# Optimization experiments

Measured on AMD Instinct MI355X. Metric: run time of the kernel, lower is better.

Reference implementation:

```python
import jax, jax.numpy as jnp
import numpy as np


def setup_inputs() -> dict:
    key = jax.random.key(0)
    k1, k2, k3, k4 = jax.random.split(key, 4)
    B, S, d_in, d_out = 4, 2048, 1024, 1024
    scale = 1.0 / np.sqrt(d_in)
    x = jax.random.normal(k1, (B, S, d_in), dtype=jnp.float32)
    # Linear weights stored as [d_in, d_out] so projection is x @ W
    Wq = jax.random.normal(k2, (d_in, d_out), dtype=jnp.float32) * scale
    Wk = jax.random.normal(k3, (d_in, d_out), dtype=jnp.float32) * scale
    Wv = jax.random.normal(k4, (d_in, d_out), dtype=jnp.float32) * scale
    return {"x": x, "Wq": Wq, "Wk": Wk, "Wv": Wv}


def reference(x, Wq, Wk, Wv):
    # QKV projections (no bias, matching qkv_bias=False)
    q = jnp.einsum("bsi,io->bso", x, Wq)
    k = jnp.einsum("bsi,io->bso", x, Wk)
    v = jnp.einsum("bsi,io->bso", x, Wv)
    d_k = k.shape[-1]
    # attn_scores = q @ k^T, causal mask (strict upper triangle -> -inf)
    scores = jnp.einsum("bqd,bkd->bqk", q, k)
    S = scores.shape[-1]
    causal = jnp.tril(jnp.ones((S, S), dtype=bool))  # True where allowed
    scores = jnp.where(causal, scores, -jnp.inf)
    attn = jax.nn.softmax(scores / jnp.sqrt(jnp.asarray(d_k, scores.dtype)), axis=-1)
    # dropout p=0.0 -> identity
    return jnp.einsum("bqk,bkd->bqd", attn, v)
```

## Files before the change

kernel.cpp:

```cpp
#include <hip/hip_runtime.h>

typedef _Float16 half8 __attribute__((ext_vector_type(8)));
typedef _Float16 half4 __attribute__((ext_vector_type(4)));
typedef float f32x4 __attribute__((ext_vector_type(4)));

#define ATT_SCALE 0.03125f
#define S_LEN 2048
#define D_DIM 1024
#define NB 4

__device__ __forceinline__ void async_cp16(const _Float16* g, _Float16* l)
{
    __builtin_amdgcn_global_load_lds(
        (const __attribute__((address_space(1))) void*)g,
        (__attribute__((address_space(3))) void*)l, 16, 0, 0);
}

__device__ __forceinline__ void gemm_core(const _Float16* __restrict__ Ag,
                                          const _Float16* __restrict__ Bg,
                                          int lda, int ldb, int ksteps,
                                          f32x4 acc[4][4])
{
    __shared__ _Float16 As[128 * 32];
    __shared__ _Float16 Bs[128 * 32];

    const int t    = threadIdx.x;
    const int wave = t >> 6;
    const int lane = t & 63;
    const int wm   = (wave >> 1) * 64;
    const int wn   = (wave & 1) * 64;
    const int lg   = lane >> 4;
    const int lr   = lane & 15;

    const int c0 = t,        r0 = c0 >> 2, h0 = (c0 & 3) * 8;
    const int c1 = 256 + t,  r1 = c1 >> 2, h1 = (c1 & 3) * 8;
    const int lb0 = (wave * 64) * 8;
    const int lb1 = (256 + wave * 64) * 8;

    const _Float16* a0p = Ag + (long)r0 * lda + h0;
    const _Float16* a1p = Ag + (long)r1 * lda + h1;
    const _Float16* b0p = Bg + (long)r0 * ldb + h0;
    const _Float16* b1p = Bg + (long)r1 * ldb + h1;

    for (int ks = 0; ks < ksteps; ++ks) {
        __syncthreads();
        async_cp16(a0p, As + lb0);
        async_cp16(a1p, As + lb1);
        async_cp16(b0p, Bs + lb0);
        async_cp16(b1p, Bs + lb1);
        __syncthreads();

        a0p += 32; a1p += 32; b0p += 32; b1p += 32;

        half8 af[4], bf[4];
#pragma unroll
        for (int i = 0; i < 4; ++i)
            af[i] = *(const half8*)&As[(wm + i * 16 + lr) * 32 + lg * 8];
#pragma unroll
        for (int j = 0; j < 4; ++j)
            bf[j] = *(const half8*)&Bs[(wn + j * 16 + lr) * 32 + lg * 8];

#pragma unroll
        for (int i = 0; i < 4; ++i)
#pragma unroll
            for (int j = 0; j < 4; ++j)
                acc[i][j] = __builtin_amdgcn_mfma_f32_16x16x32_f16(af[i], bf[j], acc[i][j], 0, 0, 0);
    }
}

__global__ void zero_sums_kernel(float* __restrict__ rs)
{
    rs[blockIdx.x * 256 + threadIdx.x] = 0.f;
}

__global__ void zero_out_kernel(float4* __restrict__ p, long n4)
{
    const float4 z = {0.f, 0.f, 0.f, 0.f};
    for (long i = (long)blockIdx.x * blockDim.x + threadIdx.x; i < n4;
         i += (long)gridDim.x * blockDim.x)
        p[i] = z;
}

__global__ void cast_x_kernel(const float* __restrict__ X, _Float16* __restrict__ Xh, int n)
{
    int i = blockIdx.x * blockDim.x + threadIdx.x;
    if (i * 4 >= n) return;
    float4 v = ((const float4*)X)[i];
    half4 h;
    h.x = (_Float16)v.x; h.y = (_Float16)v.y; h.z = (_Float16)v.z; h.w = (_Float16)v.w;
    ((half4*)Xh)[i] = h;
}

__global__ void transpose_w_kernel(const float* __restrict__ Wq,
                                   const float* __restrict__ Wk,
                                   const float* __restrict__ Wv,
                                   _Float16* __restrict__ Wt)
{
    __shared__ float tile[32][33];
    const int n0 = blockIdx.x * 32, k0 = blockIdx.y * 32, w = blockIdx.z;
    const float* Wsrc = (w == 0) ? Wq : (w == 1) ? Wk : Wv;
    _Float16* dst = Wt + (long)w * D_DIM * D_DIM;
    const int tx = threadIdx.x, ty = threadIdx.y;
#pragma unroll
    for (int j = 0; j < 4; ++j)
        tile[ty + 8 * j][tx] = Wsrc[(long)(k0 + ty + 8 * j) * D_DIM + n0 + tx];
    __syncthreads();
#pragma unroll
    for (int j = 0; j < 4; ++j)
        dst[(long)(n0 + ty + 8 * j) * D_DIM + k0 + tx] = (_Float16)tile[tx][ty + 8 * j];
}

__global__ __launch_bounds__(512, 1) void proj_kernel(const _Float16* __restrict__ Xh,
                                                      const _Float16* __restrict__ Wt,
                                                      _Float16* __restrict__ Q,
                                                      _Float16* __restrict__ K,
                                                      _Float16* __restrict__ V)
{
    __shared__ _Float16 As3[3][256 * 64];
    __shared__ _Float16 Bs3[3][128 * 64];

    const int bid = blockIdx.x;
    const int g   = (bid & 7) * 96 + (bid >> 3);
    const int w   = g >> 8;
    const int mt  = (g & 255) >> 3;
    const int nt  = g & 7;

    const int t    = threadIdx.x;
    const int wave = t >> 6;
    const int lane = t & 63;
    const int wr   = wave >> 2;
    const int wc   = wave & 3;
    const int lg   = lane >> 4;
    const int lr   = lane & 15;

    const _Float16* Ag = Xh + (long)mt * 256 * D_DIM;
    const _Float16* Bg = Wt + (long)w * D_DIM * D_DIM + (long)nt * 128 * D_DIM;

    const int rsel = lane >> 3;
    const int csel = ((lane & 7) ^ rsel) * 8;
    const int srow = wave * 8 + rsel;
    const int ldst = wave * 512;

#define STAGE_A(wb, kt2)                                                        \
    {                                                                           \
        _Pragma("unroll")                                                       \
        for (int u_ = 0; u_ < 2; ++u_)                                          \
            _Pragma("unroll")                                                   \
            for (int l_ = 0; l_ < 2; ++l_)                                      \
                async_cp16(Ag + (long)(u_ * 128 + l_ * 64 + srow) * D_DIM +      \
                               (kt2) * 64 + csel,                               \
                           As3[wb] + u_ * 8192 + l_ * 4096 + ldst);             \
    }
#define STAGE_B(wb, kt2)                                                        \
    {                                                                           \
        _Pragma("unroll")                                                       \
        for (int l_ = 0; l_ < 2; ++l_)                                          \
            async_cp16(Bg + (long)(l_ * 64 + srow) * D_DIM + (kt2) * 64 + csel, \
                       Bs3[wb] + l_ * 4096 + ldst);                             \
    }

    f32x4 acc[8][2];
#pragma unroll
    for (int i = 0; i < 8; ++i)
#pragma unroll
        for (int j = 0; j < 2; ++j) acc[i][j] = (f32x4){0.f, 0.f, 0.f, 0.f};

    STAGE_A(0, 0); STAGE_B(0, 0);
    STAGE_A(1, 1); STAGE_B(1, 1);
    asm volatile("s_waitcnt vmcnt(6)" ::: "memory");
    __builtin_amdgcn_s_barrier();

    const int cswz = (lr & 7) << 4;
    int rd = 0, wb = 2;

    for (int kt = 0; kt < 16; ++kt) {
        const char* Ab = (const char*)As3[rd];
        const char* Bb = (const char*)Bs3[rd];

        half8 bf[2][2], af[2][4];
#pragma unroll
        for (int kk = 0; kk < 2; ++kk) {
            const int cb = (kk * 64 + lg * 16) ^ cswz;
#pragma unroll
            for (int nf = 0; nf < 2; ++nf)
                bf[kk][nf] = *(const half8*)(Bb + (wc * 32 + nf * 16 + lr) * 128 + cb);
#pragma unroll
            for (int mf = 0; mf < 4; ++mf)
                af[kk][mf] = *(const half8*)(Ab + (wr * 128 + mf * 16 + lr) * 128 + cb);
        }
        if (kt < 14) STAGE_A(wb, kt + 2);
        __builtin_amdgcn_s_barrier();
        asm volatile("s_waitcnt lgkmcnt(0)" ::: "memory");
        __builtin_amdgcn_sched_barrier(0);
        __builtin_amdgcn_s_setprio(1);
#pragma unroll
        for (int kk = 0; kk < 2; ++kk)
#pragma unroll
            for (int mf = 0; mf < 4; ++mf)
#pragma unroll
                for (int nf = 0; nf < 2; ++nf)
                    acc[mf][nf] = __builtin_amdgcn_mfma_f32_16x16x32_f16(
                        af[kk][mf], bf[kk][nf], acc[mf][nf], 0, 0, 0);
        __builtin_amdgcn_s_setprio(0);
        __builtin_amdgcn_s_barrier();

        half8 a2[2][4];
#pragma unroll
        for (int kk = 0; kk < 2; ++kk) {
            const int cb = (kk * 64 + lg * 16) ^ cswz;
#pragma unroll
            for (int mf = 0; mf < 4; ++mf)
                a2[kk][mf] = *(const half8*)(Ab + (wr * 128 + (4 + mf) * 16 + lr) * 128 + cb);
        }
        if (kt < 14) STAGE_B(wb, kt + 2);
        __builtin_amdgcn_s_barrier();
        asm volatile("s_waitcnt lgkmcnt(0)" ::: "memory");
        __builtin_amdgcn_sched_barrier(0);
        __builtin_amdgcn_s_setprio(1);
#pragma unroll
        for (int kk = 0; kk < 2; ++kk)
#pragma unroll
            for (int mf = 0; mf < 4; ++mf)
#pragma unroll
                for (int nf = 0; nf < 2; ++nf)
                    acc[4 + mf][nf] = __builtin_amdgcn_mfma_f32_16x16x32_f16(
                        a2[kk][mf], bf[kk][nf], acc[4 + mf][nf], 0, 0, 0);
        __builtin_amdgcn_s_setprio(0);
        if (kt == 14)     asm volatile("s_waitcnt vmcnt(0)" ::: "memory");
        else if (kt < 14) asm volatile("s_waitcnt vmcnt(6)" ::: "memory");
        __builtin_amdgcn_s_barrier();

        rd = (rd == 2) ? 0 : rd + 1;
        wb = (wb == 2) ? 0 : wb + 1;
    }
#undef STAGE_A
#undef STAGE_B

    _Float16* C = (w == 0) ? Q : (w == 1) ? K : V;
    const long row0 = (long)mt * 256 + wr * 128 + lg * 4;
    const long col0 = (long)nt * 128 + wc * 32 + lr;
#pragma unroll
    for (int mf = 0; mf < 8; ++mf)
#pragma unroll
        for (int nf = 0; nf < 2; ++nf)
#pragma unroll
            for (int rr = 0; rr < 4; ++rr)
                C[(row0 + mf * 16 + rr) * D_DIM + col0 + nf * 16] = (_Float16)acc[mf][nf][rr];
}

__global__ __launch_bounds__(256) void transpose_v_kernel(const _Float16* __restrict__ V,
                                                          _Float16* __restrict__ Vt)
{
    __shared__ _Float16 tile[64][72];
    const int d0 = blockIdx.x * 64, s0 = blockIdx.y * 64;
    const long b = blockIdx.z;
    const _Float16* Vb = V + b * S_LEN * D_DIM;
    _Float16* Vtb = Vt + b * D_DIM * S_LEN;
    const int t = threadIdx.x;
    const int sr = t >> 3, c8 = (t & 7) * 8;

    *(half8*)&tile[sr][c8]      = *(const half8*)&Vb[(long)(s0 + sr) * D_DIM + d0 + c8];
    *(half8*)&tile[sr + 32][c8] = *(const half8*)&Vb[(long)(s0 + sr + 32) * D_DIM + d0 + c8];
    __syncthreads();

    const int dr = t >> 3, s8 = (t & 7) * 8;
    half8 o0, o1;
#pragma unroll
    for (int e = 0; e < 8; ++e) {
        o0[e] = tile[s8 + e][dr];
        o1[e] = tile[s8 + e][dr + 32];
    }
    *(half8*)&Vtb[(long)(d0 + dr) * S_LEN + s0 + s8]      = o0;
    *(half8*)&Vtb[(long)(d0 + dr + 32) * S_LEN + s0 + s8] = o1;
}

__global__ __launch_bounds__(256) void scores_exp_kernel(const _Float16* __restrict__ Q,
                                                         const _Float16* __restrict__ K,
                                                         _Float16* __restrict__ P,
                                                         float* __restrict__ row_sum)
{
    const int xcd = blockIdx.x & 7;
    const int idx = blockIdx.x >> 3;
    const int b   = idx / 17;
    const int l   = idx % 17;
    int qt, kt;
    if (l <= xcd) { qt = xcd;      kt = l; }
    else          { qt = 15 - xcd; kt = l - xcd - 1; }

    f32x4 acc[4][4];
#pragma unroll
    for (int i = 0; i < 4; ++i)
#pragma unroll
        for (int j = 0; j < 4; ++j) acc[i][j] = (f32x4){0.f, 0.f, 0.f, 0.f};

    const _Float16* Ag = Q + ((long)b * S_LEN + qt * 128) * D_DIM;
    const _Float16* Bg = K + ((long)b * S_LEN + kt * 128) * D_DIM;
    gemm_core(Ag, Bg, D_DIM, D_DIM, D_DIM / 32, acc);

    _Float16* Pb = P + (long)b * S_LEN * S_LEN;
    float* rsb = row_sum + (long)b * S_LEN;
    const int t = threadIdx.x, wave = t >> 6, lane = t & 63;
    const int wm = (wave >> 1) * 64, wn = (wave & 1) * 64;
    const int lg = lane >> 4, lr = lane & 15;
    const int row0 = qt * 128 + wm + 4 * lg;
    const int col0 = kt * 128 + wn + lr;

#pragma unroll
    for (int i = 0; i < 4; ++i) {
#pragma unroll
        for (int r = 0; r < 4; ++r) {
            const int row = row0 + i * 16 + r;
            float s = 0.f;
#pragma unroll
            for (int j = 0; j < 4; ++j) {
                const int col = col0 + j * 16;
                float p = (col <= row) ? __expf(acc[i][j][r] * ATT_SCALE) : 0.f;
                s += p;
                Pb[(long)row * S_LEN + col] = (_Float16)p;
            }
#pragma unroll
            for (int off = 1; off < 16; off <<= 1) s += __shfl_xor(s, off, 64);
            if (lr == 0) atomicAdd(&rsb[row], s);
        }
    }
}

__global__ __launch_bounds__(256) void pv_kernel(const _Float16* __restrict__ P,
                                                 const _Float16* __restrict__ Vt,
                                                 const float* __restrict__ row_sum,
                                                 float* __restrict__ O)
{
    const int xcd = blockIdx.x & 7;
    int r = blockIdx.x >> 3;
    const int b = r / 24;  r %= 24;
    const int j = r >> 3;
    const int nt = r & 7;
    const int sl = (j == 0) ? (7 - xcd) : (j == 1 ? 8 + 2 * xcd : 9 + 2 * xcd);

    int qt, k0s, ks;
    if (sl < 8) { qt = sl; k0s = 0; ks = (qt + 1) * 4; }
    else {
        const int e = sl - 8;
        qt = 8 + (e >> 1);
        ks = (qt + 1) * 2;
        k0s = (e & 1) * ks;
    }

    f32x4 acc[4][4];
#pragma unroll
    for (int i = 0; i < 4; ++i)
#pragma unroll
        for (int jj = 0; jj < 4; ++jj) acc[i][jj] = (f32x4){0.f, 0.f, 0.f, 0.f};

    const _Float16* Ag = P + ((long)b * S_LEN + qt * 128) * S_LEN + k0s * 32;
    const _Float16* Bg = Vt + (long)b * D_DIM * S_LEN + (long)nt * 128 * S_LEN + k0s * 32;
    gemm_core(Ag, Bg, S_LEN, S_LEN, ks, acc);

    float* Ob = O + (long)b * S_LEN * D_DIM;
    const float* rsb = row_sum + (long)b * S_LEN;
    const int t = threadIdx.x, wave = t >> 6, lane = t & 63;
    const int wm = (wave >> 1) * 64, wn = (wave & 1) * 64;
    const int lg = lane >> 4, lr = lane & 15;
    const long row0 = qt * 128 + wm + 4 * lg;
    const long col0 = (long)nt * 128 + wn + lr;

    if (sl < 8) {
#pragma unroll
        for (int i = 0; i < 4; ++i)
#pragma unroll
            for (int rr = 0; rr < 4; ++rr) {
                const float inv = 1.f / rsb[row0 + i * 16 + rr];
#pragma unroll
                for (int jj = 0; jj < 4; ++jj)
                    Ob[(row0 + i * 16 + rr) * D_DIM + col0 + jj * 16] = acc[i][jj][rr] * inv;
            }
    } else {
#pragma unroll
        for (int i = 0; i < 4; ++i)
#pragma unroll
            for (int rr = 0; rr < 4; ++rr) {
                const float inv = 1.f / rsb[row0 + i * 16 + rr];
#pragma unroll
                for (int jj = 0; jj < 4; ++jj)
                    atomicAdd(&Ob[(row0 + i * 16 + rr) * D_DIM + col0 + jj * 16],
                              acc[i][jj][rr] * inv);
            }
    }
}

extern "C" void kernel_launch(void* const* d_in, const int* in_sizes, int n_in,
                              void* d_out, int out_size, void* d_ws, size_t ws_size,
                              hipStream_t stream)
{
    const float* x  = (const float*)d_in[0];
    const float* Wq = (const float*)d_in[1];
    const float* Wk = (const float*)d_in[2];
    const float* Wv = (const float*)d_in[3];
    float* out = (float*)d_out;

    char* ws = (char*)d_ws;
    const long MiB = 1024 * 1024;
    _Float16* Q  = (_Float16*)(ws + 0 * MiB);
    _Float16* K  = (_Float16*)(ws + 16 * MiB);
    _Float16* V  = (_Float16*)(ws + 32 * MiB);
    _Float16* Vt = (_Float16*)(ws + 48 * MiB);
    _Float16* Xh = (_Float16*)(ws + 64 * MiB);
    _Float16* Wt = (_Float16*)(ws + 80 * MiB);
    _Float16* P  = (_Float16*)(ws + 86 * MiB);
    float*    RS = (float*)   (ws + 118 * MiB);

    const int nX = in_sizes[0];

    zero_sums_kernel<<<dim3(NB * S_LEN / 256), dim3(256), 0, stream>>>(RS);
    zero_out_kernel<<<dim3(2048), dim3(256), 0, stream>>>((float4*)out,
                                                          (long)NB * S_LEN * D_DIM / 4);
    cast_x_kernel<<<dim3((nX / 4 + 255) / 256), dim3(256), 0, stream>>>(x, Xh, nX);
    transpose_w_kernel<<<dim3(32, 32, 3), dim3(32, 8), 0, stream>>>(Wq, Wk, Wv, Wt);
    proj_kernel<<<dim3(768), dim3(512), 0, stream>>>(Xh, Wt, Q, K, V);
    transpose_v_kernel<<<dim3(16, 32, 4), dim3(256), 0, stream>>>(V, Vt);
    scores_exp_kernel<<<dim3(544), dim3(256), 0, stream>>>(Q, K, P, RS);
    pv_kernel<<<dim3(768), dim3(256), 0, stream>>>(P, Vt, RS, out);
}
```

Baseline: 189.1 us.

## Reshape projection GEMM tile from 256x128 to 128x256 with per-K-half phases

Swaps the projection kernel's block tile from 256 rows of X by 128 output columns to 128 rows by 256 columns. Each wave now computes a 64x64 sub-tile (4x4 MFMA fragments) instead of 128x32, which gives a more square register tile and better operand reuse per LDS read. The two compute phases per K-step are reorganised to split along the K halves instead of along M halves, with the B loads split into two staged halves. The tile count stays the same, but the per-wave LDS read pattern and the async-load ordering change, and the hand-tuned vmcnt waits have to stay correct with the new issue counts.

```diff
diff --git a/kernel.cpp b/kernel.cpp
--- a/kernel.cpp
+++ b/kernel.cpp
@@ -116,14 +116,14 @@
                                                       _Float16* __restrict__ K,
                                                       _Float16* __restrict__ V)
 {
-    __shared__ _Float16 As3[3][256 * 64];
-    __shared__ _Float16 Bs3[3][128 * 64];
+    __shared__ _Float16 As3[3][128 * 64];
+    __shared__ _Float16 Bs3[3][256 * 64];
 
     const int bid = blockIdx.x;
     const int g   = (bid & 7) * 96 + (bid >> 3);
     const int w   = g >> 8;
-    const int mt  = (g & 255) >> 3;
-    const int nt  = g & 7;
+    const int mt  = (g & 255) >> 2;
+    const int nt  = g & 3;
 
     const int t    = threadIdx.x;
     const int wave = t >> 6;
@@ -133,8 +133,8 @@
     const int lg   = lane >> 4;
     const int lr   = lane & 15;
 
-    const _Float16* Ag = Xh + (long)mt * 256 * D_DIM;
-    const _Float16* Bg = Wt + (long)w * D_DIM * D_DIM + (long)nt * 128 * D_DIM;
+    const _Float16* Ag = Xh + (long)mt * 128 * D_DIM;
+    const _Float16* Bg = Wt + (long)w * D_DIM * D_DIM + (long)nt * 256 * D_DIM;
 
     const int rsel = lane >> 3;
     const int csel = ((lane & 7) ^ rsel) * 8;
@@ -145,28 +145,32 @@
     {                                                                           \
         _Pragma("unroll")                                                       \
         for (int u_ = 0; u_ < 2; ++u_)                                          \
-            _Pragma("unroll")                                                   \
-            for (int l_ = 0; l_ < 2; ++l_)                                      \
-                async_cp16(Ag + (long)(u_ * 128 + l_ * 64 + srow) * D_DIM +      \
-                               (kt2) * 64 + csel,                               \
-                           As3[wb] + u_ * 8192 + l_ * 4096 + ldst);             \
-    }
-#define STAGE_B(wb, kt2)                                                        \
+            async_cp16(Ag + (long)(u_ * 64 + srow) * D_DIM + (kt2) * 64 + csel, \
+                       As3[wb] + u_ * 4096 + ldst);                             \
+    }
+#define STAGE_B01(wb, kt2)                                                      \
     {                                                                           \
         _Pragma("unroll")                                                       \
-        for (int l_ = 0; l_ < 2; ++l_)                                          \
-            async_cp16(Bg + (long)(l_ * 64 + srow) * D_DIM + (kt2) * 64 + csel, \
-                       Bs3[wb] + l_ * 4096 + ldst);                             \
-    }
-
-    f32x4 acc[8][2];
-#pragma unroll
-    for (int i = 0; i < 8; ++i)
-#pragma unroll
-        for (int j = 0; j < 2; ++j) acc[i][j] = (f32x4){0.f, 0.f, 0.f, 0.f};
-
-    STAGE_A(0, 0); STAGE_B(0, 0);
-    STAGE_A(1, 1); STAGE_B(1, 1);
+        for (int v_ = 0; v_ < 2; ++v_)                                          \
+            async_cp16(Bg + (long)(v_ * 64 + srow) * D_DIM + (kt2) * 64 + csel, \
+                       Bs3[wb] + v_ * 4096 + ldst);                             \
+    }
+#define STAGE_B23(wb, kt2)                                                      \
+    {                                                                           \
+        _Pragma("unroll")                                                       \
+        for (int v_ = 2; v_ < 4; ++v_)                                          \
+            async_cp16(Bg + (long)(v_ * 64 + srow) * D_DIM + (kt2) * 64 + csel, \
+                       Bs3[wb] + v_ * 4096 + ldst);                             \
+    }
+
+    f32x4 acc[4][4];
+#pragma unroll
+    for (int i = 0; i < 4; ++i)
+#pragma unroll
+        for (int j = 0; j < 4; ++j) acc[i][j] = (f32x4){0.f, 0.f, 0.f, 0.f};
+
+    STAGE_A(0, 0); STAGE_B01(0, 0); STAGE_B23(0, 0);
+    STAGE_A(1, 1); STAGE_B01(1, 1); STAGE_B23(1, 1);
     asm volatile("s_waitcnt vmcnt(6)" ::: "memory");
     __builtin_amdgcn_s_barrier();
 
@@ -177,72 +181,70 @@
         const char* Ab = (const char*)As3[rd];
         const char* Bb = (const char*)Bs3[rd];
 
-        half8 bf[2][2], af[2][4];
-#pragma unroll
-        for (int kk = 0; kk < 2; ++kk) {
-            const int cb = (kk * 64 + lg * 16) ^ cswz;
-#pragma unroll
-            for (int nf = 0; nf < 2; ++nf)
-                bf[kk][nf] = *(const half8*)(Bb + (wc * 32 + nf * 16 + lr) * 128 + cb);
+        {
+            const int cb = (lg * 16) ^ cswz;
+            half8 af[4], bf[4];
+#pragma unroll
+            for (int nf = 0; nf < 4; ++nf)
+                bf[nf] = *(const half8*)(Bb + (wc * 64 + nf * 16 + lr) * 128 + cb);
 #pragma unroll
             for (int mf = 0; mf < 4; ++mf)
-                af[kk][mf] = *(const half8*)(Ab + (wr * 128 + mf * 16 + lr) * 128 + cb);
+                af[mf] = *(const half8*)(Ab + (wr * 64 + mf * 16 + lr) * 128 + cb);
+            if (kt < 14) { STAGE_A(wb, kt + 2); STAGE_B01(wb, kt + 2); }
+            __builtin_amdgcn_s_barrier();
+            asm volatile("s_waitcnt lgkmcnt(0)" ::: "memory");
+            __builtin_amdgcn_sched_barrier(0);
+            __builtin_amdgcn_s_setprio(1);
+#pragma unroll
+            for (int mf = 0; mf < 4; ++mf)
+#pragma unroll
+                for (int nf = 0; nf < 4; ++nf)
+                    acc[mf][nf] = __builtin_amdgcn_mfma_f32_16x16x32_f16(
+                        af[mf], bf[nf], acc[mf][nf], 0, 0, 0);
+            __builtin_amdgcn_s_setprio(0);
+            __builtin_amdgcn_s_barrier();
         }
-        if (kt < 14) STAGE_A(wb, kt + 2);
-        __builtin_amdgcn_s_barrier();
-        asm volatile("s_waitcnt lgkmcnt(0)" ::: "memory");
-        __builtin_amdgcn_sched_barrier(0);
-        __builtin_amdgcn_s_setprio(1);
-#pragma unroll
-        for (int kk = 0; kk < 2; ++kk)
+
+        {
+            const int cb = (64 + lg * 16) ^ cswz;
+            half8 af[4], bf[4];
+#pragma unroll
+            for (int nf = 0; nf < 4; ++nf)
+                bf[nf] = *(const half8*)(Bb + (wc * 64 + nf * 16 + lr) * 128 + cb);
 #pragma unroll
             for (int mf = 0; mf < 4; ++mf)
-#pragma unroll
-                for (int nf = 0; nf < 2; ++nf)
+                af[mf] = *(const half8*)(Ab + (wr * 64 + mf * 16 + lr) * 128 + cb);
+            if (kt < 14) STAGE_B23(wb, kt + 2);
+            __builtin_amdgcn_s_barrier();
+            asm volatile("s_waitcnt lgkmcnt(0)" ::: "memory");
+            __builtin_amdgcn_sched_barrier(0);
+            __builtin_amdgcn_s_setprio(1);
+#pragma unroll
+            for (int mf = 0; mf < 4; ++mf)
+#pragma unroll
+                for (int nf = 0; nf < 4; ++nf)
                     acc[mf][nf] = __builtin_amdgcn_mfma_f32_16x16x32_f16(
-                        af[kk][mf], bf[kk][nf], acc[mf][nf], 0, 0, 0);
-        __builtin_amdgcn_s_setprio(0);
-        __builtin_amdgcn_s_barrier();
-
-        half8 a2[2][4];
-#pragma unroll
-        for (int kk = 0; kk < 2; ++kk) {
-            const int cb = (kk * 64 + lg * 16) ^ cswz;
-#pragma unroll
-            for (int mf = 0; mf < 4; ++mf)
-                a2[kk][mf] = *(const half8*)(Ab + (wr * 128 + (4 + mf) * 16 + lr) * 128 + cb);
+                        af[mf], bf[nf], acc[mf][nf], 0, 0, 0);
+            __builtin_amdgcn_s_setprio(0);
+            if (kt == 14)     asm volatile("s_waitcnt vmcnt(0)" ::: "memory");
+            else if (kt < 14) asm volatile("s_waitcnt vmcnt(6)" ::: "memory");
+            __builtin_amdgcn_s_barrier();
         }
-        if (kt < 14) STAGE_B(wb, kt + 2);
-        __builtin_amdgcn_s_barrier();
-        asm volatile("s_waitcnt lgkmcnt(0)" ::: "memory");
-        __builtin_amdgcn_sched_barrier(0);
-        __builtin_amdgcn_s_setprio(1);
-#pragma unroll
-        for (int kk = 0; kk < 2; ++kk)
-#pragma unroll
-            for (int mf = 0; mf < 4; ++mf)
-#pragma unroll
-                for (int nf = 0; nf < 2; ++nf)
-                    acc[4 + mf][nf] = __builtin_amdgcn_mfma_f32_16x16x32_f16(
-                        a2[kk][mf], bf[kk][nf], acc[4 + mf][nf], 0, 0, 0);
-        __builtin_amdgcn_s_setprio(0);
-        if (kt == 14)     asm volatile("s_waitcnt vmcnt(0)" ::: "memory");
-        else if (kt < 14) asm volatile("s_waitcnt vmcnt(6)" ::: "memory");
-        __builtin_amdgcn_s_barrier();
 
         rd = (rd == 2) ? 0 : rd + 1;
         wb = (wb == 2) ? 0 : wb + 1;
     }
 #undef STAGE_A
-#undef STAGE_B
+#undef STAGE_B01
+#undef STAGE_B23
 
     _Float16* C = (w == 0) ? Q : (w == 1) ? K : V;
-    const long row0 = (long)mt * 256 + wr * 128 + lg * 4;
-    const long col0 = (long)nt * 128 + wc * 32 + lr;
-#pragma unroll
-    for (int mf = 0; mf < 8; ++mf)
-#pragma unroll
-        for (int nf = 0; nf < 2; ++nf)
+    const long row0 = (long)mt * 128 + wr * 64 + lg * 4;
+    const long col0 = (long)nt * 256 + wc * 64 + lr;
+#pragma unroll
+    for (int mf = 0; mf < 4; ++mf)
+#pragma unroll
+        for (int nf = 0; nf < 4; ++nf)
 #pragma unroll
             for (int rr = 0; rr < 4; ++rr)
                 C[(row0 + mf * 16 + rr) * D_DIM + col0 + nf * 16] = (_Float16)acc[mf][nf][rr];
```

Result: no change. 188.1 us (-0.5%).
